# Optimization experiments

Measured on AMD Instinct MI355X. Metric: run time of the kernel, lower is better.

## Reference

```python
import jax, jax.numpy as jnp
import numpy as np

P = 1048576   # total sampled points
N = 8192      # rays
E = 8         # experts
H = 128       # expert hidden dim
TOP_K = 2
INTERVAL = 0.5      # stepsize * voxel_size_ratio
ACT_SHIFT = -4.0    # models[-1].act_shift
THRESH = 1e-4       # fast_color_thres (ndc=False)


def raw2alpha(d):
    # Raw2Alpha: alpha = 1 - exp(-softplus(density + act_shift) * interval)
    return 1.0 - jnp.exp(-jax.nn.softplus(d + ACT_SHIFT) * INTERVAL)


def alphas2weights(alpha, ray_id, n_rays):
    # Sequential per-ray transmittance: w_j = alpha_j * prod_{k<j in ray}(1 - alpha_k)
    la = jnp.log1p(-jnp.clip(alpha, 0.0, 1.0 - 1e-6))      # [P], <= 0
    cum = jnp.cumsum(la)
    excl = cum - la                                          # exclusive cumsum, nonincreasing
    # offset per ray = excl at first point of the (sorted) segment == segment max
    offset = jax.ops.segment_max(excl, ray_id, num_segments=n_rays)
    T = jnp.exp(excl - offset[ray_id])                       # transmittance before each point
    weights = alpha * T
    alphainv_last = jnp.exp(jax.ops.segment_sum(la, ray_id, num_segments=n_rays))
    return weights, alphainv_last


def setup_inputs() -> dict:
    key = jax.random.key(0)
    ks = jax.random.split(key, 12)
    s = 0.3  # weight scale keeping activations in a sane range
    return {
        "ray_pts": jax.random.uniform(ks[0], (P, 3), dtype=jnp.float32),
        "viewdirs": jax.random.normal(ks[1], (N, 3), dtype=jnp.float32),
        "bg": jnp.ones((3,), dtype=jnp.float32),
        "Wd1": jax.random.normal(ks[2], (3, H), dtype=jnp.float32) * s,
        "bd1": jnp.zeros((H,), dtype=jnp.float32),
        "Wd2": jax.random.normal(ks[3], (H, 1), dtype=jnp.float32) * s,
        "Wg": jax.random.normal(ks[4], (6, E), dtype=jnp.float32) * s,
        "We1": jax.random.normal(ks[5], (E, 6, H), dtype=jnp.float32) * s,
        "be1": jnp.zeros((E, H), dtype=jnp.float32),
        "Wrgb": jax.random.normal(ks[6], (E, H, 3), dtype=jnp.float32) * s,
        "Walpha": jax.random.normal(ks[7], (E, H, 1), dtype=jnp.float32) * s,
        "ray_id": jnp.sort(jax.random.randint(ks[8], (P,), 0, N)).astype(jnp.int32),
    }


def reference(ray_pts, viewdirs, bg, Wd1, bd1, Wd2, Wg, We1, be1, Wrgb, Walpha, ray_id):
    # --- density grid query + activation ---
    hd = jax.nn.relu(ray_pts @ Wd1 + bd1)                    # [P,H]
    density = (hd @ Wd2)[:, 0]                               # [P]
    alpha0 = raw2alpha(density)
    # filter low density (zeroing alpha == dropping the point from the cumprod)
    alpha0 = jnp.where(alpha0 > THRESH, alpha0, 0.0)
    w0, _ = alphas2weights(alpha0, ray_id, N)
    # filter low transmittance (w0 <= THRESH also covers alpha0 == 0)
    keep = w0 > THRESH                                        # [P] bool

    # --- gate: softmax over experts, top-k, renormalize ---
    x = jnp.concatenate([ray_pts, viewdirs[ray_id]], axis=-1)  # [P,6]
    probs = jax.nn.softmax(x @ Wg, axis=-1)                    # [P,E]
    vals, idx = jax.lax.top_k(probs, TOP_K)                    # [P,K]
    vals = vals / jnp.sum(vals, axis=-1, keepdims=True)        # top_k > 1
    g = jnp.sum(vals[..., None] * jax.nn.one_hot(idx, E, dtype=vals.dtype), axis=1)  # [P,E]
    g = g * keep[:, None].astype(g.dtype)

    # --- per-expert radiance / alpha, mixed by gate weights ---
    rgb = jnp.zeros((ray_pts.shape[0], 3), dtype=ray_pts.dtype)
    alpha_mix = jnp.zeros((ray_pts.shape[0],), dtype=ray_pts.dtype)
    for e in range(E):  # fixed small expert count
        h = jax.nn.relu(x @ We1[e] + be1[e])                   # [P,H]
        rgb_e = jax.nn.sigmoid(h @ Wrgb[e])                    # [P,3]
        a_e = raw2alpha((h @ Walpha[e])[:, 0])                 # [P]
        rgb = rgb + g[:, e:e + 1] * rgb_e
        alpha_mix = alpha_mix + g[:, e] * a_e

    # --- composite: Alphas2Weights + segment_coo sum + background ---
    w, alphainv_last = alphas2weights(alpha_mix, ray_id, N)
    rgb_marched = jax.ops.segment_sum(w[:, None] * rgb, ray_id, num_segments=N)
    rgb_marched = rgb_marched + alphainv_last[:, None] * bg
    return rgb_marched
```

## Files before the change

### kernel.cpp

```cpp
#include <hip/hip_runtime.h>

#define PTOT   1048576
#define NRAYS  8192
#define THRESH 1e-4f

typedef float F2 __attribute__((ext_vector_type(2)));

__device__ __forceinline__ F2 f2splat(float s){ F2 r; r.x = s; r.y = s; return r; }
__device__ __forceinline__ F2 f2fma(F2 a, float b, F2 c){
    return __builtin_elementwise_fma(a, f2splat(b), c);
}
__device__ __forceinline__ float raw2alpha_f(float d){
    return 1.0f - rsqrtf(1.0f + __expf(d - 4.0f));
}

__global__ __launch_bounds__(256) void k_point(
    const float* __restrict__ pts, const float* __restrict__ vdirs,
    const int* __restrict__ ray_id,
    const float* __restrict__ Wd1, const float* __restrict__ bd1,
    const float* __restrict__ Wd2, const float* __restrict__ Wg,
    float* __restrict__ alpha0, float* __restrict__ g0a, int* __restrict__ eea,
    float4* __restrict__ vd, int* __restrict__ ray_off)
{
    __shared__ float4 WD4[128];
    __shared__ float  WD2s[128];
    __shared__ float  WGs[8][6];
    int t = threadIdx.x;
    if (t < 128){
        WD4[t] = make_float4(Wd1[t], Wd1[128+t], Wd1[256+t], bd1[t]);
        WD2s[t] = Wd2[t];
    }
    if (t < 48) WGs[t & 7][t >> 3] = Wg[t];
    __syncthreads();

    int base = blockIdx.x * 2048 + t;
    F2 px[4], py[4], pz[4], vx[4], vy[4], vz[4], dens[4];
    int rid0[4], rid1[4];
    #pragma unroll
    for (int q=0;q<4;q++){
        int p0 = base + (2*q)*256, p1 = p0 + 256;
        px[q] = (F2){pts[3*p0],   pts[3*p1]};
        py[q] = (F2){pts[3*p0+1], pts[3*p1+1]};
        pz[q] = (F2){pts[3*p0+2], pts[3*p1+2]};
        int r0 = ray_id[p0], r1 = ray_id[p1];
        rid0[q] = r0; rid1[q] = r1;
        vx[q] = (F2){vdirs[3*r0],   vdirs[3*r1]};
        vy[q] = (F2){vdirs[3*r0+1], vdirs[3*r1+1]};
        vz[q] = (F2){vdirs[3*r0+2], vdirs[3*r1+2]};
        dens[q] = f2splat(0.f);
    }
    #pragma unroll
    for (int q=0;q<4;q++){
        int p0 = base + (2*q)*256, p1 = p0 + 256;
        vd[p0] = make_float4(vx[q].x, vy[q].x, vz[q].x, 0.f);
        vd[p1] = make_float4(vx[q].y, vy[q].y, vz[q].y, 0.f);
        int prev0 = (p0 == 0) ? -1 : ray_id[p0-1];
        if (prev0 != rid0[q]) for (int r=prev0+1; r<=rid0[q]; ++r) ray_off[r] = p0;
        int prev1 = ray_id[p1-1];
        if (prev1 != rid1[q]) for (int r=prev1+1; r<=rid1[q]; ++r) ray_off[r] = p1;
        if (p1 == PTOT-1) for (int r=rid1[q]+1; r<=NRAYS; ++r) ray_off[r] = PTOT;
    }
    #pragma unroll 2
    for (int i=0;i<128;i++){
        float4 w = WD4[i]; float w2 = WD2s[i];
        #pragma unroll
        for (int q=0;q<4;q++){
            F2 h = f2fma(px[q], w.x, f2fma(py[q], w.y, f2fma(pz[q], w.z, f2splat(w.w))));
            h = __builtin_elementwise_max(h, f2splat(0.f));
            dens[q] = f2fma(h, w2, dens[q]);
        }
    }
    #pragma unroll
    for (int q=0;q<4;q++){
        float a0 = raw2alpha_f(dens[q].x);
        float a1 = raw2alpha_f(dens[q].y);
        alpha0[base + (2*q)*256]   = (a0 > THRESH) ? a0 : 0.f;
        alpha0[base + (2*q+1)*256] = (a1 > THRESH) ? a1 : 0.f;
    }
    float m0[8], m1[8]; int i0[8], i1[8];
    #pragma unroll
    for (int j=0;j<8;j++){ m0[j]=-3.0e38f; m1[j]=-3.0e38f; i0[j]=0; i1[j]=0; }
    for (int e=0;e<8;e++){
        float w0=WGs[e][0],w1=WGs[e][1],w2=WGs[e][2],w3=WGs[e][3],w4=WGs[e][4],w5=WGs[e][5];
        #pragma unroll
        for (int q=0;q<4;q++){
            F2 l = f2fma(px[q],w0, f2fma(py[q],w1, f2fma(pz[q],w2,
                   f2fma(vx[q],w3, f2fma(vy[q],w4,
                   __builtin_elementwise_fma(vz[q], f2splat(w5), f2splat(0.f)))))));
            int j0 = 2*q, j1 = 2*q+1;
            float lx = l.x, ly = l.y;
            if (lx > m0[j0]){ m1[j0]=m0[j0]; i1[j0]=i0[j0]; m0[j0]=lx; i0[j0]=e; }
            else if (lx > m1[j0]){ m1[j0]=lx; i1[j0]=e; }
            if (ly > m0[j1]){ m1[j1]=m0[j1]; i1[j1]=i0[j1]; m0[j1]=ly; i0[j1]=e; }
            else if (ly > m1[j1]){ m1[j1]=ly; i1[j1]=e; }
        }
    }
    #pragma unroll
    for (int j=0;j<8;j++){
        float g0 = __fdividef(1.0f, 1.0f + __expf(m1[j]-m0[j]));
        g0a[base + j*256] = g0;
        eea[base + j*256] = i0[j] | (i1[j] << 8);
    }
}

__global__ __launch_bounds__(256) void k_scan0(const float* __restrict__ alpha0,
                                               const int* __restrict__ eea,
                                               const int* __restrict__ ray_off,
                                               unsigned char* __restrict__ keep,
                                               int* __restrict__ cntA)
{
    __shared__ int wcs[4][8];
    int t = threadIdx.x, lane = t & 63, w = t >> 6;
    int wid = blockIdx.x*4 + w;
    int c[8];
    #pragma unroll
    for (int e=0;e<8;e++) c[e]=0;
    int s = ray_off[wid], e = ray_off[wid+1];
    float carry = 1.f;
    for (int ch = s; ch < e; ch += 64){
        int p = ch + lane;
        bool in = p < e;
        float a = in ? alpha0[p] : 0.f;
        int  ee = in ? eea[p] : 0;
        float incl = 1.f - a;
        #pragma unroll
        for (int d=1; d<64; d<<=1){ float tt = __shfl_up(incl, d); if (lane >= d) incl *= tt; }
        float excl = __shfl_up(incl, 1); if (lane == 0) excl = 1.f;
        float w0 = a * carry * excl;
        int k = (in && w0 > THRESH) ? 1 : 0;
        if (in) keep[p] = (unsigned char)k;
        int e0 = ee & 255, e1 = (ee >> 8) & 255;
        #pragma unroll
        for (int x=0;x<8;x++){
            unsigned long long m0 = __ballot(k && e0==x);
            unsigned long long m1 = __ballot(k && e1==x);
            c[x] += __popcll(m0) + __popcll(m1);
        }
        carry *= __shfl(incl, 63);
    }
    if (lane == 0){
        #pragma unroll
        for (int x=0;x<8;x++) wcs[w][x] = c[x];
    }
    __syncthreads();
    if (t < 8){
        int sum = wcs[0][t]+wcs[1][t]+wcs[2][t]+wcs[3][t];
        if (sum) atomicAdd(&cntA[t], sum);
    }
}

__global__ __launch_bounds__(256) void k_fill(const unsigned char* __restrict__ keep,
                                              const float* __restrict__ g0a,
                                              const int* __restrict__ eea,
                                              const int* __restrict__ cntA,
                                              int* __restrict__ curA,
                                              int2* __restrict__ ent)
{
    __shared__ int wc[4][8];
    __shared__ int wb[4][8];
    __shared__ int sOff[8];
    int t = threadIdx.x, lane = t & 63, w = t >> 6;
    unsigned long long lt = (1ull << lane) - 1ull;
    int base = blockIdx.x * 2048;

    int c[8];
    #pragma unroll
    for (int e=0;e<8;e++) c[e]=0;
    for (int j=0;j<8;j++){
        int p = base + (j*4 + w)*64 + lane;
        int k = keep[p];
        int ee = eea[p];
        int e0 = ee & 255, e1 = (ee >> 8) & 255;
        #pragma unroll
        for (int e=0;e<8;e++){
            unsigned long long m0 = __ballot(k && e0==e);
            unsigned long long m1 = __ballot(k && e1==e);
            c[e] += __popcll(m0) + __popcll(m1);
        }
    }
    if (lane == 0){
        #pragma unroll
        for (int e=0;e<8;e++) wc[w][e] = c[e];
    }
    if (t == 0){
        int acc = 0;
        for (int e=0;e<8;e++){ sOff[e] = acc; acc += cntA[e]; }
    }
    __syncthreads();
    if (t < 8){
        int tot = wc[0][t]+wc[1][t]+wc[2][t]+wc[3][t];
        int b = sOff[t] + (tot ? atomicAdd(&curA[t], tot) : 0);
        wb[0][t] = b; b += wc[0][t];
        wb[1][t] = b; b += wc[1][t];
        wb[2][t] = b; b += wc[2][t];
        wb[3][t] = b;
    }
    __syncthreads();

    int cur[8];
    #pragma unroll
    for (int e=0;e<8;e++) cur[e] = wb[w][e];
    for (int j=0;j<8;j++){
        int p = base + (j*4 + w)*64 + lane;
        int k = keep[p];
        float g0 = g0a[p];
        int ee = eea[p];
        int e0 = ee & 255, e1 = (ee >> 8) & 255;
        #pragma unroll
        for (int e=0;e<8;e++){
            unsigned long long m0 = __ballot(k && e0==e);
            unsigned long long m1 = __ballot(k && e1==e);
            if (k && e0==e)
                ent[cur[e] + __popcll(m0 & lt)] = make_int2(p, __float_as_int(g0));
            if (k && e1==e)
                ent[cur[e] + __popcll(m0) + __popcll(m1 & lt)] =
                    make_int2(p | (1 << 30), __float_as_int(1.0f - g0));
            cur[e] += __popcll(m0) + __popcll(m1);
        }
    }
}

__global__ __launch_bounds__(256) void k_expert(
    const int2* __restrict__ ent, const int* __restrict__ cntA,
    const float* __restrict__ pts, const float4* __restrict__ vd,
    const float* __restrict__ We1, const float* __restrict__ be1,
    const float* __restrict__ Wrgb, const float* __restrict__ Walpha,
    float4* __restrict__ res)
{
    int e    = blockIdx.x >> 9;
    int bi   = blockIdx.x & 511;
    int base = bi * 2048;

    __shared__ float4 WA[128];
    __shared__ float4 WB[128];
    __shared__ float4 WC[128];
    __shared__ int sSeg[2];
    int t = threadIdx.x;
    if (t < 128){
        const float* w = We1 + e*768;
        WA[t] = make_float4(w[t], w[128+t], w[256+t], w[384+t]);
        WB[t] = make_float4(w[512+t], w[640+t], be1[e*128+t], Walpha[e*128+t]);
        const float* wr = Wrgb + e*384 + 3*t;
        WC[t] = make_float4(wr[0], wr[1], wr[2], 0.f);
    }
    if (t == 0){
        int acc = 0;
        for (int i=0;i<e;i++) acc += cntA[i];
        sSeg[0] = acc; sSeg[1] = cntA[e];
    }
    __syncthreads();
    int n = sSeg[1];
    if (base >= n) return;
    const int2* eb = ent + sSeg[0];

    F2 x0[4],x1[4],x2[4],x3[4],x4[4],x5[4];
    F2 ar[4],ag[4],ab[4],aa[4];
    #pragma unroll
    for (int pr=0;pr<4;pr++){
        int idx0 = base + t + (2*pr)*256, idx1 = idx0 + 256;
        int2 r0 = (idx0 < n) ? eb[idx0] : make_int2(0,0);
        int2 r1 = (idx1 < n) ? eb[idx1] : make_int2(0,0);
        int p0 = r0.x & 0x0FFFFFFF, p1 = r1.x & 0x0FFFFFFF;
        x0[pr] = (F2){pts[3*p0],   pts[3*p1]};
        x1[pr] = (F2){pts[3*p0+1], pts[3*p1+1]};
        x2[pr] = (F2){pts[3*p0+2], pts[3*p1+2]};
        float4 v0 = vd[p0], v1 = vd[p1];
        x3[pr] = (F2){v0.x, v1.x};
        x4[pr] = (F2){v0.y, v1.y};
        x5[pr] = (F2){v0.z, v1.z};
        ar[pr] = f2splat(0.f); ag[pr] = f2splat(0.f);
        ab[pr] = f2splat(0.f); aa[pr] = f2splat(0.f);
    }
    #pragma unroll 2
    for (int i=0;i<128;i++){
        float4 wa = WA[i], wb = WB[i], wc = WC[i];
        #pragma unroll
        for (int pr=0;pr<4;pr++){
            F2 h = f2fma(x0[pr],wa.x, f2fma(x1[pr],wa.y, f2fma(x2[pr],wa.z,
                   f2fma(x3[pr],wa.w, f2fma(x4[pr],wb.x, f2fma(x5[pr],wb.y,
                   f2splat(wb.z)))))));
            h = __builtin_elementwise_max(h, f2splat(0.f));
            ar[pr] = f2fma(h, wc.x, ar[pr]);
            ag[pr] = f2fma(h, wc.y, ag[pr]);
            ab[pr] = f2fma(h, wc.z, ab[pr]);
            aa[pr] = f2fma(h, wb.w, aa[pr]);
        }
    }
    #pragma unroll
    for (int pr=0;pr<4;pr++){
        #pragma unroll
        for (int sel=0; sel<2; sel++){
            int idx = base + t + (2*pr+sel)*256;
            if (idx < n){
                int2 rec = eb[idx];
                float vr = sel ? ar[pr].y : ar[pr].x;
                float vg = sel ? ag[pr].y : ag[pr].x;
                float vb = sel ? ab[pr].y : ab[pr].x;
                float va = sel ? aa[pr].y : aa[pr].x;
                float sr = __fdividef(1.0f, 1.0f + __expf(-vr));
                float sg = __fdividef(1.0f, 1.0f + __expf(-vg));
                float sb = __fdividef(1.0f, 1.0f + __expf(-vb));
                float a  = raw2alpha_f(va);
                float g  = __int_as_float(rec.y);
                int pp   = rec.x & 0x0FFFFFFF;
                int slot = ((unsigned)rec.x) >> 30;
                res[2*(size_t)pp + slot] = make_float4(g*sr, g*sg, g*sb, g*a);
            }
        }
    }
}

__global__ __launch_bounds__(256) void k_scan1(const float4* __restrict__ res,
                                               const unsigned char* __restrict__ keep,
                                               const int* __restrict__ ray_off,
                                               const float* __restrict__ bg,
                                               float* __restrict__ out)
{
    int wid  = (blockIdx.x*blockDim.x + threadIdx.x) >> 6;
    int lane = threadIdx.x & 63;
    if (wid >= NRAYS) return;
    int s = ray_off[wid], e = ray_off[wid+1];
    float carry = 1.f;
    float accx = 0.f, accy = 0.f, accz = 0.f;
    for (int c = s; c < e; c += 64){
        int p = c + lane;
        float4 v = make_float4(0.f,0.f,0.f,0.f);
        if (p < e && keep[p]){
            float4 v0 = res[2*(size_t)p];
            float4 v1 = res[2*(size_t)p + 1];
            v = make_float4(v0.x+v1.x, v0.y+v1.y, v0.z+v1.z, v0.w+v1.w);
        }
        float a = v.w;
        float incl = 1.f - a;
        #pragma unroll
        for (int d=1; d<64; d<<=1){ float tt = __shfl_up(incl, d); if (lane >= d) incl *= tt; }
        float excl = __shfl_up(incl, 1); if (lane == 0) excl = 1.f;
        float w = a * carry * excl;
        accx = fmaf(w, v.x, accx);
        accy = fmaf(w, v.y, accy);
        accz = fmaf(w, v.z, accz);
        carry *= __shfl(incl, 63);
    }
    #pragma unroll
    for (int d=32; d; d>>=1){
        accx += __shfl_xor(accx, d);
        accy += __shfl_xor(accy, d);
        accz += __shfl_xor(accz, d);
    }
    if (lane == 0){
        out[3*wid+0] = accx + carry*bg[0];
        out[3*wid+1] = accy + carry*bg[1];
        out[3*wid+2] = accz + carry*bg[2];
    }
}

extern "C" void kernel_launch(void* const* d_in, const int* in_sizes, int n_in,
                              void* d_out, int out_size, void* d_ws, size_t ws_size,
                              hipStream_t stream)
{
    const float* pts    = (const float*)d_in[0];
    const float* vdirs  = (const float*)d_in[1];
    const float* bg     = (const float*)d_in[2];
    const float* Wd1    = (const float*)d_in[3];
    const float* bd1    = (const float*)d_in[4];
    const float* Wd2    = (const float*)d_in[5];
    const float* Wg     = (const float*)d_in[6];
    const float* We1    = (const float*)d_in[7];
    const float* be1    = (const float*)d_in[8];
    const float* Wrgb   = (const float*)d_in[9];
    const float* Walpha = (const float*)d_in[10];
    const int*   ray_id = (const int*)d_in[11];
    float* out = (float*)d_out;

    char* ws = (char*)d_ws;
    size_t off = 0;
    float* alpha0        = (float*)(ws + off); off += (size_t)PTOT*4;
    float* g0a           = (float*)(ws + off); off += (size_t)PTOT*4;
    int*   eea           = (int*)  (ws + off); off += (size_t)PTOT*4;
    unsigned char* keep  = (unsigned char*)(ws + off); off += (size_t)PTOT;
    int*   ray_off       = (int*)  (ws + off); off += 33024;
    int*   cntA          = (int*)  (ws + off); off += 256;
    int*   curA          = (int*)  (ws + off); off += 256;
    off = (off + 255) & ~(size_t)255;
    float4* vd           = (float4*)(ws + off); off += (size_t)PTOT*16;
    int2*  ent           = (int2*) (ws + off); off += (size_t)2*PTOT*8;
    float4* res          = (float4*)(ws + off); off += ((size_t)2*PTOT+2)*16;

    hipMemsetAsync(cntA, 0, 512, stream);

    k_point <<<PTOT/2048, 256, 0, stream>>>(pts, vdirs, ray_id, Wd1, bd1, Wd2, Wg,
                                            alpha0, g0a, eea, vd, ray_off);
    k_scan0 <<<NRAYS/4, 256, 0, stream>>>(alpha0, eea, ray_off, keep, cntA);
    k_fill  <<<PTOT/2048, 256, 0, stream>>>(keep, g0a, eea, cntA, curA, ent);
    k_expert<<<8*512, 256, 0, stream>>>(ent, cntA, pts, vd,
                                        We1, be1, Wrgb, Walpha, res);
    k_scan1 <<<NRAYS*64/256, 256, 0, stream>>>(res, keep, ray_off, bg, out);
}
```

Before: 249.9 us.

## Pre-pack expert weights and read them directly in a grid-strided expert kernel

A new prep kernel packs each expert's first-layer weights, bias, alpha and rgb weights into a contiguous float4 array. The expert kernel then reads weights straight from global memory (uniform loads) instead of staging them in shared memory with a barrier, and drops its serial prefix sum over cntA. Blocks per expert go from 512 to 256, each thread handles 4 points instead of 8, and a grid-stride loop covers the rest. Entry records are kept in registers rather than reloaded. The aim is to cut per-block setup and LDS traffic and to launch fewer idle blocks, at the cost of an extra launch and per-iteration global or scalar weight loads.

```diff
diff --git a/kernel.cpp b/kernel.cpp
--- a/kernel.cpp
+++ b/kernel.cpp
@@ -12,6 +12,22 @@
 }
 __device__ __forceinline__ float raw2alpha_f(float d){
     return 1.0f - rsqrtf(1.0f + __expf(d - 4.0f));
+}
+
+__global__ __launch_bounds__(128) void k_prep(
+    const float* __restrict__ We1, const float* __restrict__ be1,
+    const float* __restrict__ Wrgb, const float* __restrict__ Walpha,
+    float* __restrict__ Wt)
+{
+    int e = blockIdx.x, t = threadIdx.x;
+    const float* w = We1 + e*768;
+    float* dst = Wt + (size_t)(e*128 + t)*12;
+    dst[0]  = w[t];       dst[1]  = w[128+t];   dst[2]  = w[256+t]; dst[3] = w[384+t];
+    dst[4]  = w[512+t];   dst[5]  = w[640+t];
+    dst[6]  = be1[e*128+t];
+    dst[7]  = Walpha[e*128+t];
+    const float* wr = Wrgb + e*384 + 3*t;
+    dst[8]  = wr[0];      dst[9]  = wr[1];      dst[10] = wr[2];    dst[11] = 0.f;
 }
 
 __global__ __launch_bounds__(256) void k_point(
@@ -223,88 +239,79 @@
 __global__ __launch_bounds__(256) void k_expert(
     const int2* __restrict__ ent, const int* __restrict__ cntA,
     const float* __restrict__ pts, const float4* __restrict__ vd,
-    const float* __restrict__ We1, const float* __restrict__ be1,
-    const float* __restrict__ Wrgb, const float* __restrict__ Walpha,
+    const float4* __restrict__ Wt4,
     float4* __restrict__ res)
 {
-    int e    = blockIdx.x >> 9;
-    int bi   = blockIdx.x & 511;
-    int base = bi * 2048;
-
-    __shared__ float4 WA[128];
-    __shared__ float4 WB[128];
-    __shared__ float4 WC[128];
-    __shared__ int sSeg[2];
+    int e  = blockIdx.x >> 8;
+    int bi = blockIdx.x & 255;
+    int s0 = 0, n = 0;
+    #pragma unroll
+    for (int i=0;i<8;i++){
+        int c = cntA[i];
+        s0 += (i < e) ? c : 0;
+        n   = (i == e) ? c : n;
+    }
+    if (bi*1024 >= n) return;
+    const int2* eb = ent + s0;
+    const float4* W = Wt4 + (size_t)e * 384;
     int t = threadIdx.x;
-    if (t < 128){
-        const float* w = We1 + e*768;
-        WA[t] = make_float4(w[t], w[128+t], w[256+t], w[384+t]);
-        WB[t] = make_float4(w[512+t], w[640+t], be1[e*128+t], Walpha[e*128+t]);
-        const float* wr = Wrgb + e*384 + 3*t;
-        WC[t] = make_float4(wr[0], wr[1], wr[2], 0.f);
-    }
-    if (t == 0){
-        int acc = 0;
-        for (int i=0;i<e;i++) acc += cntA[i];
-        sSeg[0] = acc; sSeg[1] = cntA[e];
-    }
-    __syncthreads();
-    int n = sSeg[1];
-    if (base >= n) return;
-    const int2* eb = ent + sSeg[0];
-
-    F2 x0[4],x1[4],x2[4],x3[4],x4[4],x5[4];
-    F2 ar[4],ag[4],ab[4],aa[4];
-    #pragma unroll
-    for (int pr=0;pr<4;pr++){
-        int idx0 = base + t + (2*pr)*256, idx1 = idx0 + 256;
-        int2 r0 = (idx0 < n) ? eb[idx0] : make_int2(0,0);
-        int2 r1 = (idx1 < n) ? eb[idx1] : make_int2(0,0);
-        int p0 = r0.x & 0x0FFFFFFF, p1 = r1.x & 0x0FFFFFFF;
-        x0[pr] = (F2){pts[3*p0],   pts[3*p1]};
-        x1[pr] = (F2){pts[3*p0+1], pts[3*p1+1]};
-        x2[pr] = (F2){pts[3*p0+2], pts[3*p1+2]};
-        float4 v0 = vd[p0], v1 = vd[p1];
-        x3[pr] = (F2){v0.x, v1.x};
-        x4[pr] = (F2){v0.y, v1.y};
-        x5[pr] = (F2){v0.z, v1.z};
-        ar[pr] = f2splat(0.f); ag[pr] = f2splat(0.f);
-        ab[pr] = f2splat(0.f); aa[pr] = f2splat(0.f);
-    }
-    #pragma unroll 2
-    for (int i=0;i<128;i++){
-        float4 wa = WA[i], wb = WB[i], wc = WC[i];
-        #pragma unroll
-        for (int pr=0;pr<4;pr++){
-            F2 h = f2fma(x0[pr],wa.x, f2fma(x1[pr],wa.y, f2fma(x2[pr],wa.z,
-                   f2fma(x3[pr],wa.w, f2fma(x4[pr],wb.x, f2fma(x5[pr],wb.y,
-                   f2splat(wb.z)))))));
-            h = __builtin_elementwise_max(h, f2splat(0.f));
-            ar[pr] = f2fma(h, wc.x, ar[pr]);
-            ag[pr] = f2fma(h, wc.y, ag[pr]);
-            ab[pr] = f2fma(h, wc.z, ab[pr]);
-            aa[pr] = f2fma(h, wb.w, aa[pr]);
-        }
-    }
-    #pragma unroll
-    for (int pr=0;pr<4;pr++){
-        #pragma unroll
-        for (int sel=0; sel<2; sel++){
-            int idx = base + t + (2*pr+sel)*256;
-            if (idx < n){
-                int2 rec = eb[idx];
-                float vr = sel ? ar[pr].y : ar[pr].x;
-                float vg = sel ? ag[pr].y : ag[pr].x;
-                float vb = sel ? ab[pr].y : ab[pr].x;
-                float va = sel ? aa[pr].y : aa[pr].x;
-                float sr = __fdividef(1.0f, 1.0f + __expf(-vr));
-                float sg = __fdividef(1.0f, 1.0f + __expf(-vg));
-                float sb = __fdividef(1.0f, 1.0f + __expf(-vb));
-                float a  = raw2alpha_f(va);
-                float g  = __int_as_float(rec.y);
-                int pp   = rec.x & 0x0FFFFFFF;
-                int slot = ((unsigned)rec.x) >> 30;
-                res[2*(size_t)pp + slot] = make_float4(g*sr, g*sg, g*sb, g*a);
+
+    for (int base = bi*1024; base < n; base += 256*1024){
+        F2 x0[2],x1[2],x2[2],x3[2],x4[2],x5[2];
+        F2 ar[2],ag[2],ab[2],aa[2];
+        int2 rr[4];
+        #pragma unroll
+        for (int pr=0;pr<2;pr++){
+            int idx0 = base + t + pr*512, idx1 = idx0 + 256;
+            int2 r0 = (idx0 < n) ? eb[idx0] : make_int2(0,0);
+            int2 r1 = (idx1 < n) ? eb[idx1] : make_int2(0,0);
+            rr[2*pr] = r0; rr[2*pr+1] = r1;
+            int p0 = r0.x & 0x0FFFFFFF, p1 = r1.x & 0x0FFFFFFF;
+            x0[pr] = (F2){pts[3*p0],   pts[3*p1]};
+            x1[pr] = (F2){pts[3*p0+1], pts[3*p1+1]};
+            x2[pr] = (F2){pts[3*p0+2], pts[3*p1+2]};
+            float4 v0 = vd[p0], v1 = vd[p1];
+            x3[pr] = (F2){v0.x, v1.x};
+            x4[pr] = (F2){v0.y, v1.y};
+            x5[pr] = (F2){v0.z, v1.z};
+            ar[pr] = f2splat(0.f); ag[pr] = f2splat(0.f);
+            ab[pr] = f2splat(0.f); aa[pr] = f2splat(0.f);
+        }
+        #pragma unroll 2
+        for (int i=0;i<128;i++){
+            float4 wa = W[3*i], wb = W[3*i+1], wc = W[3*i+2];
+            #pragma unroll
+            for (int pr=0;pr<2;pr++){
+                F2 h = f2fma(x0[pr],wa.x, f2fma(x1[pr],wa.y, f2fma(x2[pr],wa.z,
+                       f2fma(x3[pr],wa.w, f2fma(x4[pr],wb.x, f2fma(x5[pr],wb.y,
+                       f2splat(wb.z)))))));
+                h = __builtin_elementwise_max(h, f2splat(0.f));
+                ar[pr] = f2fma(h, wc.x, ar[pr]);
+                ag[pr] = f2fma(h, wc.y, ag[pr]);
+                ab[pr] = f2fma(h, wc.z, ab[pr]);
+                aa[pr] = f2fma(h, wb.w, aa[pr]);
+            }
+        }
+        #pragma unroll
+        for (int pr=0;pr<2;pr++){
+            #pragma unroll
+            for (int sel=0; sel<2; sel++){
+                int idx = base + t + pr*512 + sel*256;
+                if (idx < n){
+                    int2 rec = rr[2*pr+sel];
+                    float vr = sel ? ar[pr].y : ar[pr].x;
+                    float vg = sel ? ag[pr].y : ag[pr].x;
+                    float vb = sel ? ab[pr].y : ab[pr].x;
+                    float va = sel ? aa[pr].y : aa[pr].x;
+                    float sr = __fdividef(1.0f, 1.0f + __expf(-vr));
+                    float sg = __fdividef(1.0f, 1.0f + __expf(-vg));
+                    float sb = __fdividef(1.0f, 1.0f + __expf(-vb));
+                    float a  = raw2alpha_f(va);
+                    float g  = __int_as_float(rec.y);
+                    int pp   = rec.x & 0x0FFFFFFF;
+                    int slot = ((unsigned)rec.x) >> 30;
+                    res[2*(size_t)pp + slot] = make_float4(g*sr, g*sg, g*sb, g*a);
+                }
             }
         }
     }
@@ -385,14 +392,16 @@
     float4* vd           = (float4*)(ws + off); off += (size_t)PTOT*16;
     int2*  ent           = (int2*) (ws + off); off += (size_t)2*PTOT*8;
     float4* res          = (float4*)(ws + off); off += ((size_t)2*PTOT+2)*16;
+    off = (off + 255) & ~(size_t)255;
+    float* Wt            = (float*)(ws + off); off += 8*128*12*4;
 
     hipMemsetAsync(cntA, 0, 512, stream);
 
+    k_prep  <<<8, 128, 0, stream>>>(We1, be1, Wrgb, Walpha, Wt);
     k_point <<<PTOT/2048, 256, 0, stream>>>(pts, vdirs, ray_id, Wd1, bd1, Wd2, Wg,
                                             alpha0, g0a, eea, vd, ray_off);
     k_scan0 <<<NRAYS/4, 256, 0, stream>>>(alpha0, eea, ray_off, keep, cntA);
     k_fill  <<<PTOT/2048, 256, 0, stream>>>(keep, g0a, eea, cntA, curA, ent);
-    k_expert<<<8*512, 256, 0, stream>>>(ent, cntA, pts, vd,
-                                        We1, be1, Wrgb, Walpha, res);
+    k_expert<<<8*256, 256, 0, stream>>>(ent, cntA, pts, vd, (const float4*)Wt, res);
     k_scan1 <<<NRAYS*64/256, 256, 0, stream>>>(res, keep, ray_off, bg, out);
 }
```

Result: slower. 286.0 us (+14.4%).

## Pack point and viewdir features into expert entries to remove gather indirection

Applied to the files above, without the earlier changes.

The fill kernel now writes a full 32-byte entry per (point, expert) holding position, view direction, gate weight and packed index. This replaces the 8-byte index/gate record, and the expert kernel reads it contiguously instead of gathering from pts and the per-point viewdir buffer. The vd buffer write in k_point is removed, and the workspace is aliased so res reuses the alpha0/g0a/eea region. The cost is four times more bytes written and read for entries, in exchange for coalesced loads and no indirect gathers in k_expert.

```diff
diff --git a/kernel.cpp b/kernel.cpp
--- a/kernel.cpp
+++ b/kernel.cpp
@@ -20,7 +20,7 @@
     const float* __restrict__ Wd1, const float* __restrict__ bd1,
     const float* __restrict__ Wd2, const float* __restrict__ Wg,
     float* __restrict__ alpha0, float* __restrict__ g0a, int* __restrict__ eea,
-    float4* __restrict__ vd, int* __restrict__ ray_off)
+    int* __restrict__ ray_off)
 {
     __shared__ float4 WD4[128];
     __shared__ float  WD2s[128];
@@ -52,8 +52,6 @@
     #pragma unroll
     for (int q=0;q<4;q++){
         int p0 = base + (2*q)*256, p1 = p0 + 256;
-        vd[p0] = make_float4(vx[q].x, vy[q].x, vz[q].x, 0.f);
-        vd[p1] = make_float4(vx[q].y, vy[q].y, vz[q].y, 0.f);
         int prev0 = (p0 == 0) ? -1 : ray_id[p0-1];
         if (prev0 != rid0[q]) for (int r=prev0+1; r<=rid0[q]; ++r) ray_off[r] = p0;
         int prev1 = ray_id[p1-1];
@@ -154,7 +152,10 @@
                                               const int* __restrict__ eea,
                                               const int* __restrict__ cntA,
                                               int* __restrict__ curA,
-                                              int2* __restrict__ ent)
+                                              const float* __restrict__ pts,
+                                              const int* __restrict__ ray_id,
+                                              const float* __restrict__ vdirs,
+                                              float4* __restrict__ ent4)
 {
     __shared__ int wc[4][8];
     __shared__ int wb[4][8];
@@ -205,24 +206,32 @@
         int k = keep[p];
         float g0 = g0a[p];
         int ee = eea[p];
+        float x = pts[3*p], y = pts[3*p+1], z = pts[3*p+2];
+        int r = ray_id[p];
+        float vx = vdirs[3*r], vy = vdirs[3*r+1], vz = vdirs[3*r+2];
         int e0 = ee & 255, e1 = (ee >> 8) & 255;
         #pragma unroll
         for (int e=0;e<8;e++){
             unsigned long long m0 = __ballot(k && e0==e);
             unsigned long long m1 = __ballot(k && e1==e);
-            if (k && e0==e)
-                ent[cur[e] + __popcll(m0 & lt)] = make_int2(p, __float_as_int(g0));
-            if (k && e1==e)
-                ent[cur[e] + __popcll(m0) + __popcll(m1 & lt)] =
-                    make_int2(p | (1 << 30), __float_as_int(1.0f - g0));
+            if (k && e0==e){
+                int kk = cur[e] + __popcll(m0 & lt);
+                ent4[2*(size_t)kk]   = make_float4(x, y, z, vx);
+                ent4[2*(size_t)kk+1] = make_float4(vy, vz, g0, __int_as_float(p));
+            }
+            if (k && e1==e){
+                int kk = cur[e] + __popcll(m0) + __popcll(m1 & lt);
+                ent4[2*(size_t)kk]   = make_float4(x, y, z, vx);
+                ent4[2*(size_t)kk+1] = make_float4(vy, vz, 1.0f - g0,
+                                                   __int_as_float(p | (1 << 30)));
+            }
             cur[e] += __popcll(m0) + __popcll(m1);
         }
     }
 }
 
 __global__ __launch_bounds__(256) void k_expert(
-    const int2* __restrict__ ent, const int* __restrict__ cntA,
-    const float* __restrict__ pts, const float4* __restrict__ vd,
+    const float4* __restrict__ ent4, const int* __restrict__ cntA,
     const float* __restrict__ We1, const float* __restrict__ be1,
     const float* __restrict__ Wrgb, const float* __restrict__ Walpha,
     float4* __restrict__ res)
@@ -251,23 +260,25 @@
     __syncthreads();
     int n = sSeg[1];
     if (base >= n) return;
-    const int2* eb = ent + sSeg[0];
+    const float4* eb = ent4 + 2*(size_t)sSeg[0];
 
     F2 x0[4],x1[4],x2[4],x3[4],x4[4],x5[4];
     F2 ar[4],ag[4],ab[4],aa[4];
+    float gg[8]; int bb[8];
     #pragma unroll
     for (int pr=0;pr<4;pr++){
         int idx0 = base + t + (2*pr)*256, idx1 = idx0 + 256;
-        int2 r0 = (idx0 < n) ? eb[idx0] : make_int2(0,0);
-        int2 r1 = (idx1 < n) ? eb[idx1] : make_int2(0,0);
-        int p0 = r0.x & 0x0FFFFFFF, p1 = r1.x & 0x0FFFFFFF;
-        x0[pr] = (F2){pts[3*p0],   pts[3*p1]};
-        x1[pr] = (F2){pts[3*p0+1], pts[3*p1+1]};
-        x2[pr] = (F2){pts[3*p0+2], pts[3*p1+2]};
-        float4 v0 = vd[p0], v1 = vd[p1];
-        x3[pr] = (F2){v0.x, v1.x};
-        x4[pr] = (F2){v0.y, v1.y};
-        x5[pr] = (F2){v0.z, v1.z};
+        float4 a0 = make_float4(0,0,0,0), b0 = a0, a1 = a0, b1 = a0;
+        if (idx0 < n){ a0 = eb[2*idx0]; b0 = eb[2*idx0+1]; }
+        if (idx1 < n){ a1 = eb[2*idx1]; b1 = eb[2*idx1+1]; }
+        x0[pr] = (F2){a0.x, a1.x};
+        x1[pr] = (F2){a0.y, a1.y};
+        x2[pr] = (F2){a0.z, a1.z};
+        x3[pr] = (F2){a0.w, a1.w};
+        x4[pr] = (F2){b0.x, b1.x};
+        x5[pr] = (F2){b0.y, b1.y};
+        gg[2*pr] = b0.z;  gg[2*pr+1] = b1.z;
+        bb[2*pr] = __float_as_int(b0.w); bb[2*pr+1] = __float_as_int(b1.w);
         ar[pr] = f2splat(0.f); ag[pr] = f2splat(0.f);
         ab[pr] = f2splat(0.f); aa[pr] = f2splat(0.f);
     }
@@ -292,7 +303,6 @@
         for (int sel=0; sel<2; sel++){
             int idx = base + t + (2*pr+sel)*256;
             if (idx < n){
-                int2 rec = eb[idx];
                 float vr = sel ? ar[pr].y : ar[pr].x;
                 float vg = sel ? ag[pr].y : ag[pr].x;
                 float vb = sel ? ab[pr].y : ab[pr].x;
@@ -301,9 +311,10 @@
                 float sg = __fdividef(1.0f, 1.0f + __expf(-vg));
                 float sb = __fdividef(1.0f, 1.0f + __expf(-vb));
                 float a  = raw2alpha_f(va);
-                float g  = __int_as_float(rec.y);
-                int pp   = rec.x & 0x0FFFFFFF;
-                int slot = ((unsigned)rec.x) >> 30;
+                float g  = gg[2*pr+sel];
+                int bits = bb[2*pr+sel];
+                int pp   = bits & 0x0FFFFFFF;
+                int slot = ((unsigned)bits) >> 30;
                 res[2*(size_t)pp + slot] = make_float4(g*sr, g*sg, g*sb, g*a);
             }
         }
@@ -374,25 +385,27 @@
 
     char* ws = (char*)d_ws;
     size_t off = 0;
-    float* alpha0        = (float*)(ws + off); off += (size_t)PTOT*4;
-    float* g0a           = (float*)(ws + off); off += (size_t)PTOT*4;
-    int*   eea           = (int*)  (ws + off); off += (size_t)PTOT*4;
     unsigned char* keep  = (unsigned char*)(ws + off); off += (size_t)PTOT;
     int*   ray_off       = (int*)  (ws + off); off += 33024;
     int*   cntA          = (int*)  (ws + off); off += 256;
     int*   curA          = (int*)  (ws + off); off += 256;
     off = (off + 255) & ~(size_t)255;
-    float4* vd           = (float4*)(ws + off); off += (size_t)PTOT*16;
-    int2*  ent           = (int2*) (ws + off); off += (size_t)2*PTOT*8;
-    float4* res          = (float4*)(ws + off); off += ((size_t)2*PTOT+2)*16;
+    size_t offA = off;
+    float* alpha0        = (float*)(ws + offA);
+    float* g0a           = (float*)(ws + offA + (size_t)PTOT*4);
+    int*   eea           = (int*)  (ws + offA + (size_t)PTOT*8);
+    float4* res          = (float4*)(ws + offA);
+    size_t resBytes      = ((size_t)2*PTOT + 2) * 16;
+    size_t offE          = (offA + resBytes + 255) & ~(size_t)255;
+    float4* ent4         = (float4*)(ws + offE);
 
     hipMemsetAsync(cntA, 0, 512, stream);
 
     k_point <<<PTOT/2048, 256, 0, stream>>>(pts, vdirs, ray_id, Wd1, bd1, Wd2, Wg,
-                                            alpha0, g0a, eea, vd, ray_off);
+                                            alpha0, g0a, eea, ray_off);
     k_scan0 <<<NRAYS/4, 256, 0, stream>>>(alpha0, eea, ray_off, keep, cntA);
-    k_fill  <<<PTOT/2048, 256, 0, stream>>>(keep, g0a, eea, cntA, curA, ent);
-    k_expert<<<8*512, 256, 0, stream>>>(ent, cntA, pts, vd,
-                                        We1, be1, Wrgb, Walpha, res);
+    k_fill  <<<PTOT/2048, 256, 0, stream>>>(keep, g0a, eea, cntA, curA,
+                                            pts, ray_id, vdirs, ent4);
+    k_expert<<<8*512, 256, 0, stream>>>(ent4, cntA, We1, be1, Wrgb, Walpha, res);
     k_scan1 <<<NRAYS*64/256, 256, 0, stream>>>(res, keep, ray_off, bg, out);
 }
```

New measurement: 259.1 us. 1.04x slower.
